# Kernel optimization log

Hardware: AMD Instinct MI355X
Metric: run time of the kernel (lower is better)

Reference implementation:

```python
import jax, jax.numpy as jnp
import numpy as np

N_NODES = 100000
N_EDGES = 1600000
N_GRAPHS = 64
H = 150
PASSES = 4


def setup_inputs() -> dict:
    key = jax.random.key(0)
    ks = jax.random.split(key, 16)
    s = 0.082  # ~1/sqrt(150), torch default init scale
    nodes = jax.random.normal(ks[0], (N_NODES, H), dtype=jnp.float32)
    src = jax.random.randint(ks[1], (N_EDGES,), 0, N_NODES, dtype=jnp.int32)
    dst = jax.random.randint(ks[2], (N_EDGES,), 0, N_NODES, dtype=jnp.int32)
    graph_ids = jnp.sort(jax.random.randint(ks[3], (N_NODES,), 0, N_GRAPHS, dtype=jnp.int32))
    u = lambda k, sh: jax.random.uniform(k, sh, dtype=jnp.float32, minval=-s, maxval=s)
    return {
        'nodes': nodes, 'src': src, 'dst': dst, 'graph_ids': graph_ids,
        'w_ih': u(ks[4], (3 * H, H)), 'w_hh': u(ks[5], (3 * H, H)),
        'b_ih': u(ks[6], (3 * H,)), 'b_hh': u(ks[7], (3 * H,)),
        'fc1_w': u(ks[8], (80, H)), 'fc1_b': u(ks[9], (80,)),
        'fc2_w': u(ks[10], (80, 80)), 'fc2_b': u(ks[11], (80,)),
        'fcl_w': u(ks[12], (10, 80)), 'fcl_b': u(ks[13], (10,)),
    }


def _gru_cell(x, h, w_ih, w_hh, b_ih, b_hh):
    # torch.nn.GRUCell semantics
    gi = x @ w_ih.T + b_ih  # [N, 3H]
    gh = h @ w_hh.T + b_hh
    i_r, i_z, i_n = jnp.split(gi, 3, axis=-1)
    h_r, h_z, h_n = jnp.split(gh, 3, axis=-1)
    r = jax.nn.sigmoid(i_r + h_r)
    z = jax.nn.sigmoid(i_z + h_z)
    n = jnp.tanh(i_n + r * h_n)
    return (1.0 - z) * n + z * h


def reference(nodes, src, dst, graph_ids, w_ih, w_hh, b_ih, b_hh,
              fc1_w, fc1_b, fc2_w, fc2_b, fcl_w, fcl_b):
    h = nodes
    for _ in range(PASSES):
        # incoming[v] = sum of h[u] over edges u->v (collect_incomingPrime)
        incoming = jax.ops.segment_sum(h[src], dst, num_segments=N_NODES)
        h = _gru_cell(incoming, h, w_ih, w_hh, b_ih, b_hh)
    # per-graph readout: sum node states, log, nan->0, relu
    g = jax.ops.segment_sum(h, graph_ids, num_segments=N_GRAPHS)  # [G, H]
    g = jnp.log(g)
    g = jnp.where(jnp.isnan(g), 0.0, g)
    g = jax.nn.relu(g)  # relu(-inf) = 0, matches torch
    x = jax.nn.leaky_relu(g @ fc1_w.T + fc1_b)
    x = jax.nn.leaky_relu(x @ fc2_w.T + fc2_b)
    return x @ fcl_w.T + fcl_b  # [G, 10]
```

## Files before the change

kernel.cpp:

```cpp
#include <hip/hip_runtime.h>

#define N_NODES 100000
#define N_EDGES 1600000
#define N_GRAPHS 64
#define HDIM 150
#define PASSES 4
#define MROWS_PAD 100032
#define SCAN_NBLK 391

typedef __attribute__((ext_vector_type(8))) short bf16x8;
typedef __attribute__((ext_vector_type(4))) float f32x4;

__device__ __forceinline__ ushort bf16_rne(float x) {
  uint u = __float_as_uint(x);
  u += 0x7FFFu + ((u >> 16) & 1u);
  return (ushort)(u >> 16);
}
__device__ __forceinline__ float bf16f(ushort h) { return __uint_as_float(((uint)h) << 16); }

__global__ void hist_kernel(const int* __restrict__ dst, int* __restrict__ counts, int n) {
  int i = blockIdx.x * blockDim.x + threadIdx.x;
  if (i < n) atomicAdd(&counts[dst[i]], 1);
}

__global__ __launch_bounds__(256) void scan1_kernel(const int* __restrict__ counts,
                                                    int* __restrict__ partials) {
  int i = blockIdx.x * 256 + threadIdx.x;
  int v = (i < N_NODES) ? counts[i] : 0;
#pragma unroll
  for (int o = 32; o; o >>= 1) v += __shfl_down(v, o);
  __shared__ int ws4[4];
  if ((threadIdx.x & 63) == 0) ws4[threadIdx.x >> 6] = v;
  __syncthreads();
  if (threadIdx.x == 0) partials[blockIdx.x] = ws4[0] + ws4[1] + ws4[2] + ws4[3];
}

__global__ __launch_bounds__(512) void scan2_kernel(int* __restrict__ partials,
                                                    int* __restrict__ row_start) {
  __shared__ int s[512];
  int t = threadIdx.x;
  int v = (t < SCAN_NBLK) ? partials[t] : 0;
  s[t] = v;
  __syncthreads();
  for (int o = 1; o < 512; o <<= 1) {
    int u = (t >= o) ? s[t - o] : 0;
    __syncthreads();
    s[t] += u;
    __syncthreads();
  }
  if (t < SCAN_NBLK) partials[t] = s[t] - v;
  if (t == 0) row_start[N_NODES] = s[511];
}

__global__ __launch_bounds__(256) void scan3_kernel(const int* __restrict__ counts,
    const int* __restrict__ partials, int* __restrict__ row_start, int* __restrict__ cursor) {
  __shared__ int s[256];
  int t = threadIdx.x, i = blockIdx.x * 256 + t;
  int v = (i < N_NODES) ? counts[i] : 0;
  s[t] = v;
  __syncthreads();
  for (int o = 1; o < 256; o <<= 1) {
    int u = (t >= o) ? s[t - o] : 0;
    __syncthreads();
    s[t] += u;
    __syncthreads();
  }
  if (i < N_NODES) {
    int ex = s[t] - v + partials[blockIdx.x];
    row_start[i] = ex; cursor[i] = ex;
  }
}

__global__ void fill_kernel(const int* __restrict__ src, const int* __restrict__ dst,
                            int* __restrict__ cursor, int* __restrict__ csr_src, int n) {
  int i = blockIdx.x * blockDim.x + threadIdx.x;
  if (i < n) {
    int pos = atomicAdd(&cursor[dst[i]], 1);
    csr_src[pos] = src[i];
  }
}

__global__ void wbuild_kernel(const float* __restrict__ wih, const float* __restrict__ whh,
                              ushort* __restrict__ Whi, ushort* __restrict__ Wlo) {
  int idx = blockIdx.x * 256 + threadIdx.x;
  if (idx >= 960 * 160) return;
  int n = idx / 160, k = idx - n * 160;
  int ch = n / 160, dd = n - ch * 160;
  float v = 0.f;
  if (dd < HDIM && k < HDIM)
    v = (ch < 3) ? wih[(ch * HDIM + dd) * HDIM + k] : whh[((ch - 3) * HDIM + dd) * HDIM + k];
  ushort hi = bf16_rne(v);
  ushort lo = bf16_rne(v - bf16f(hi));
  Whi[idx] = hi; Wlo[idx] = lo;
}

__global__ __launch_bounds__(256) void segsum_kernel(const float* __restrict__ h, const int hstride,
    const int* __restrict__ row_start, const int* __restrict__ csr_src,
    ushort* __restrict__ Xhi, ushort* __restrict__ Xlo) {
  int node = blockIdx.x * 4 + (threadIdx.x >> 6);
  if (node >= N_NODES) return;
  int lane = threadIdx.x & 63;
  int b = row_start[node], e = row_start[node + 1];
  int cnt = e - b;
  float a0 = 0.f, a1 = 0.f, a2 = 0.f;
  const bool l22 = lane < 22;

  for (int base = 0; base < cnt; base += 64) {
    const int nb = min(64, cnt - base);
    int myidx = (base + lane < cnt) ? csr_src[b + base + lane] : 0;
    int jj = 0;
    for (; jj + 4 <= nb; jj += 4) {
      const int s0 = __shfl(myidx, jj);
      const int s1 = __shfl(myidx, jj + 1);
      const int s2 = __shfl(myidx, jj + 2);
      const int s3 = __shfl(myidx, jj + 3);
      const float* r0 = h + (size_t)s0 * hstride;
      const float* r1 = h + (size_t)s1 * hstride;
      const float* r2 = h + (size_t)s2 * hstride;
      const float* r3 = h + (size_t)s3 * hstride;
      float v00 = r0[lane],      v10 = r1[lane],      v20 = r2[lane],      v30 = r3[lane];
      float v01 = r0[lane + 64], v11 = r1[lane + 64], v21 = r2[lane + 64], v31 = r3[lane + 64];
      float v02 = 0.f, v12 = 0.f, v22 = 0.f, v32 = 0.f;
      if (l22) {
        v02 = r0[lane + 128]; v12 = r1[lane + 128];
        v22 = r2[lane + 128]; v32 = r3[lane + 128];
      }
      a0 += (v00 + v10) + (v20 + v30);
      a1 += (v01 + v11) + (v21 + v31);
      a2 += (v02 + v12) + (v22 + v32);
    }
    for (; jj < nb; ++jj) {
      const int s0 = __shfl(myidx, jj);
      const float* r0 = h + (size_t)s0 * hstride;
      a0 += r0[lane];
      a1 += r0[lane + 64];
      if (l22) a2 += r0[lane + 128];
    }
  }

  int basep = node * 160;
  ushort h0 = bf16_rne(a0), l0 = bf16_rne(a0 - bf16f(h0));
  ushort h1 = bf16_rne(a1), l1 = bf16_rne(a1 - bf16f(h1));
  Xhi[basep + lane] = h0; Xlo[basep + lane] = l0;
  Xhi[basep + 64 + lane] = h1; Xlo[basep + 64 + lane] = l1;
  if (lane < 32) {
    ushort h2 = 0, l2 = 0;
    if (l22) { h2 = bf16_rne(a2); l2 = bf16_rne(a2 - bf16f(h2)); }
    Xhi[basep + 128 + lane] = h2; Xlo[basep + 128 + lane] = l2;
  }
}

__global__ __launch_bounds__(256) void gru_mfma_kernel(
    const ushort* __restrict__ Xhi, const ushort* __restrict__ Xlo,
    const float* __restrict__ hcur, const int hstride,
    const ushort* __restrict__ Whi, const ushort* __restrict__ Wlo,
    const float* __restrict__ bih, const float* __restrict__ bhh,
    float* __restrict__ hnext) {
  __shared__ ushort smem[2][8192];
  const int flat = blockIdx.x;
  const int xcd = flat & 7;
  const int q = flat >> 3;
  const int dblk = q % 5;
  const int mblk = (q / 5) * 8 + xcd;
  if (mblk >= 1563) return;

  const int tid = threadIdx.x;
  const int w = tid >> 6;
  const int l = tid & 63;
  const int c16 = l & 15;
  const int koct = l >> 4;

  const int sr = tid >> 2;
  const int so = tid & 3;
  const int sop = so ^ ((sr >> 1) & 3);
  const int gm = mblk * 64 + sr;
  const bool rowok = gm < N_NODES;
  const int g_off = gm * 160 + so * 8;
  const int lds_w_off = sr * 64 + sop * 16;

  const int hi_b = (w < 2) ? 0 : 2;
  const int dt = w & 1;
  const int ch0 = (w < 2) ? 0 : 3;
  const int nbase = dblk * 32 + dt * 16 + c16;

  f32x4 acc[3][4];
#pragma unroll
  for (int a = 0; a < 3; ++a)
#pragma unroll
    for (int b = 0; b < 4; ++b) acc[a][b] = (f32x4){0.f, 0.f, 0.f, 0.f};

  auto loadH = [&](int kc, float* hv) {
    const int kb = kc * 32 + so * 8;
    const float* hrow = hcur + (size_t)gm * hstride + kb;
#pragma unroll
    for (int e = 0; e < 8; e += 2) {
      float x0 = 0.f, x1 = 0.f;
      if (rowok) {
        if (kb + e + 1 < HDIM) { float2 v2 = *(const float2*)(hrow + e); x0 = v2.x; x1 = v2.y; }
        else if (kb + e < HDIM) { x0 = hrow[e]; }
      }
      hv[e] = x0; hv[e + 1] = x1;
    }
  };
  auto writeH = [&](int buf, const float* hv) {
    bf16x8 vh, vl;
#pragma unroll
    for (int e = 0; e < 8; ++e) {
      ushort u = bf16_rne(hv[e]);
      vh[e] = (short)u;
      vl[e] = (short)bf16_rne(hv[e] - bf16f(u));
    }
    *(bf16x8*)((char*)smem + buf * 16384 + 2 * 4096 + lds_w_off) = vh;
    *(bf16x8*)((char*)smem + buf * 16384 + 3 * 4096 + lds_w_off) = vl;
  };

  {
    bf16x8 x0 = *(const bf16x8*)(Xhi + g_off);
    bf16x8 x1 = *(const bf16x8*)(Xlo + g_off);
    float hv[8];
    loadH(0, hv);
    *(bf16x8*)((char*)smem + 0 * 4096 + lds_w_off) = x0;
    *(bf16x8*)((char*)smem + 1 * 4096 + lds_w_off) = x1;
    writeH(0, hv);
  }
  __syncthreads();

#pragma unroll
  for (int kc = 0; kc < 5; ++kc) {
    const int cur = kc & 1;
    bf16x8 nX0, nX1;
    float nhv[8];
    if (kc < 4) {
      nX0 = *(const bf16x8*)(Xhi + g_off + (kc + 1) * 32);
      nX1 = *(const bf16x8*)(Xlo + g_off + (kc + 1) * 32);
      loadH(kc + 1, nhv);
    }
    bf16x8 ahi[4], alo[4];
#pragma unroll
    for (int mt = 0; mt < 4; ++mt) {
      const int r = mt * 16 + c16;
      const int ob = (koct ^ ((r >> 1) & 3)) * 16;
      ahi[mt] = *(const bf16x8*)((char*)smem + cur * 16384 + hi_b * 4096 + r * 64 + ob);
      alo[mt] = *(const bf16x8*)((char*)smem + cur * 16384 + (hi_b + 1) * 4096 + r * 64 + ob);
    }
    bf16x8 bhi[3], blo[3];
#pragma unroll
    for (int cl = 0; cl < 3; ++cl) {
      const int wo = ((ch0 + cl) * 160 + nbase) * 160 + kc * 32 + koct * 8;
      bhi[cl] = *(const bf16x8*)(Whi + wo);
      blo[cl] = *(const bf16x8*)(Wlo + wo);
    }
#pragma unroll
    for (int cl = 0; cl < 3; ++cl)
#pragma unroll
      for (int mt = 0; mt < 4; ++mt)
        acc[cl][mt] = __builtin_amdgcn_mfma_f32_16x16x32_bf16(ahi[mt], bhi[cl], acc[cl][mt], 0, 0, 0);
#pragma unroll
    for (int cl = 0; cl < 3; ++cl)
#pragma unroll
      for (int mt = 0; mt < 4; ++mt)
        acc[cl][mt] = __builtin_amdgcn_mfma_f32_16x16x32_bf16(ahi[mt], blo[cl], acc[cl][mt], 0, 0, 0);
#pragma unroll
    for (int cl = 0; cl < 3; ++cl)
#pragma unroll
      for (int mt = 0; mt < 4; ++mt)
        acc[cl][mt] = __builtin_amdgcn_mfma_f32_16x16x32_bf16(alo[mt], bhi[cl], acc[cl][mt], 0, 0, 0);
    if (kc < 4) {
      const int nb = cur ^ 1;
      *(bf16x8*)((char*)smem + nb * 16384 + 0 * 4096 + lds_w_off) = nX0;
      *(bf16x8*)((char*)smem + nb * 16384 + 1 * 4096 + lds_w_off) = nX1;
      writeH(nb, nhv);
    }
    __syncthreads();
  }

  float* eps = (float*)smem;
  if (w >= 2) {
    const int wi = w - 2;
#pragma unroll
    for (int cl = 0; cl < 3; ++cl)
#pragma unroll
      for (int mt = 0; mt < 4; ++mt)
        *(f32x4*)&eps[(((wi * 3 + cl) * 4 + mt) * 64 + l) * 4] = acc[cl][mt];
  }
  __syncthreads();
  if (w < 2) {
    const int d = dblk * 32 + dt * 16 + c16;
    if (d < HDIM) {
      const float bir = bih[d], biz = bih[HDIM + d], bin = bih[2 * HDIM + d];
      const float bhr = bhh[d], bhz = bhh[HDIM + d], bhn = bhh[2 * HDIM + d];
#pragma unroll
      for (int mt = 0; mt < 4; ++mt) {
        const int mb = mblk * 64 + mt * 16 + koct * 4;
        f32x4 hr4 = *(const f32x4*)&eps[(((dt * 3 + 0) * 4 + mt) * 64 + l) * 4];
        f32x4 hz4 = *(const f32x4*)&eps[(((dt * 3 + 1) * 4 + mt) * 64 + l) * 4];
        f32x4 hn4 = *(const f32x4*)&eps[(((dt * 3 + 2) * 4 + mt) * 64 + l) * 4];
#pragma unroll
        for (int j = 0; j < 4; ++j) {
          const int m = mb + j;
          if (m < N_NODES) {
            const float r = 1.f / (1.f + __expf(-(acc[0][mt][j] + bir + hr4[j] + bhr)));
            const float z = 1.f / (1.f + __expf(-(acc[1][mt][j] + biz + hz4[j] + bhz)));
            const float na = acc[2][mt][j] + bin + r * (hn4[j] + bhn);
            const float nn = 1.f - 2.f / (__expf(2.f * na) + 1.f);
            const float ho = hcur[(size_t)m * hstride + d];
            hnext[m * 160 + d] = (1.f - z) * nn + z * ho;
          }
        }
      }
    }
  }
}

__global__ __launch_bounds__(64) void graph_accum_kernel(const float* __restrict__ h,
    const int* __restrict__ gids, float* __restrict__ gacc) {
  const int lane = threadIdx.x;
  const int nb = gridDim.x;
  int chunk = (N_NODES + nb - 1) / nb;
  int b = blockIdx.x * chunk, e = min(b + chunk, N_NODES);
  if (b >= e) return;
  float a0 = 0.f, a1 = 0.f, a2 = 0.f;
  int cur = gids[b];
  for (int i = b; i < e; ++i) {
    int gid = gids[i];
    if (gid != cur) {
      atomicAdd(&gacc[cur * HDIM + lane], a0);
      atomicAdd(&gacc[cur * HDIM + lane + 64], a1);
      if (lane < 22) atomicAdd(&gacc[cur * HDIM + lane + 128], a2);
      a0 = a1 = a2 = 0.f; cur = gid;
    }
    const float* hr = h + (size_t)i * 160;
    a0 += hr[lane]; a1 += hr[lane + 64];
    if (lane < 22) a2 += hr[lane + 128];
  }
  atomicAdd(&gacc[cur * HDIM + lane], a0);
  atomicAdd(&gacc[cur * HDIM + lane + 64], a1);
  if (lane < 22) atomicAdd(&gacc[cur * HDIM + lane + 128], a2);
}

__global__ __launch_bounds__(192) void readout_kernel(const float* __restrict__ gacc,
    const float* __restrict__ fc1w, const float* __restrict__ fc1b,
    const float* __restrict__ fc2w, const float* __restrict__ fc2b,
    const float* __restrict__ fclw, const float* __restrict__ fclb,
    float* __restrict__ out) {
  __shared__ float x0[HDIM];
  __shared__ float y1[80];
  __shared__ float y2[80];
  int g = blockIdx.x, t = threadIdx.x;
  if (t < HDIM) {
    float v = logf(gacc[g * HDIM + t]);
    if (v != v) v = 0.f;
    x0[t] = fmaxf(v, 0.f);
  }
  __syncthreads();
  if (t < 80) {
    float s = fc1b[t];
    for (int k = 0; k < HDIM; ++k) s += x0[k] * fc1w[t * HDIM + k];
    y1[t] = (s > 0.f) ? s : 0.01f * s;
  }
  __syncthreads();
  if (t < 80) {
    float s = fc2b[t];
    for (int k = 0; k < 80; ++k) s += y1[k] * fc2w[t * 80 + k];
    y2[t] = (s > 0.f) ? s : 0.01f * s;
  }
  __syncthreads();
  if (t < 10) {
    float s = fclb[t];
    for (int k = 0; k < 80; ++k) s += y2[k] * fclw[t * 80 + k];
    out[g * 10 + t] = s;
  }
}

extern "C" void kernel_launch(void* const* d_in, const int* in_sizes, int n_in,
                              void* d_out, int out_size, void* d_ws, size_t ws_size,
                              hipStream_t stream) {
  const float* nodes = (const float*)d_in[0];
  const int* src = (const int*)d_in[1];
  const int* dst = (const int*)d_in[2];
  const int* gids = (const int*)d_in[3];
  const float* wih = (const float*)d_in[4];
  const float* whh = (const float*)d_in[5];
  const float* bih = (const float*)d_in[6];
  const float* bhh = (const float*)d_in[7];
  const float* fc1w = (const float*)d_in[8];
  const float* fc1b = (const float*)d_in[9];
  const float* fc2w = (const float*)d_in[10];
  const float* fc2b = (const float*)d_in[11];
  const float* fclw = (const float*)d_in[12];
  const float* fclb = (const float*)d_in[13];
  float* out = (float*)d_out;

  char* wsp = (char*)d_ws;
  size_t off = 0;
  auto carve = [&](size_t bytes) {
    void* p = wsp + off;
    off += (bytes + 255) & ~(size_t)255;
    return p;
  };
  int* counts   = (int*)carve((size_t)N_NODES * 4);
  int* rowstart = (int*)carve((size_t)(N_NODES + 1) * 4);
  int* cursor   = (int*)carve((size_t)N_NODES * 4);
  int* partials = (int*)carve((size_t)512 * 4);
  int* csr      = (int*)carve((size_t)N_EDGES * 4);
  ushort* Xhi   = (ushort*)carve((size_t)MROWS_PAD * 160 * 2);
  ushort* Xlo   = (ushort*)carve((size_t)MROWS_PAD * 160 * 2);
  float* hA     = (float*)carve((size_t)MROWS_PAD * 160 * 4);
  float* hB     = (float*)carve((size_t)MROWS_PAD * 160 * 4);
  ushort* Whi   = (ushort*)carve((size_t)960 * 160 * 2);
  ushort* Wlo   = (ushort*)carve((size_t)960 * 160 * 2);
  float* gacc   = (float*)carve((size_t)N_GRAPHS * HDIM * 4);
  (void)ws_size; (void)in_sizes; (void)n_in; (void)out_size;

  hipMemsetAsync(counts, 0, (size_t)N_NODES * 4, stream);
  hipMemsetAsync(gacc, 0, (size_t)N_GRAPHS * HDIM * 4, stream);

  hist_kernel<<<(N_EDGES + 255) / 256, 256, 0, stream>>>(dst, counts, N_EDGES);
  scan1_kernel<<<SCAN_NBLK, 256, 0, stream>>>(counts, partials);
  scan2_kernel<<<1, 512, 0, stream>>>(partials, rowstart);
  scan3_kernel<<<SCAN_NBLK, 256, 0, stream>>>(counts, partials, rowstart, cursor);
  fill_kernel<<<(N_EDGES + 255) / 256, 256, 0, stream>>>(src, dst, cursor, csr, N_EDGES);
  wbuild_kernel<<<600, 256, 0, stream>>>(wih, whh, Whi, Wlo);

  const float* hcur = nodes;
  int hstride = HDIM;
  float* hnxt = hA;
  for (int p = 0; p < PASSES; ++p) {
    segsum_kernel<<<25000, 256, 0, stream>>>(hcur, hstride, rowstart, csr, Xhi, Xlo);
    gru_mfma_kernel<<<7840, 256, 0, stream>>>(
        Xhi, Xlo, hcur, hstride, Whi, Wlo, bih, bhh, hnxt);
    hcur = hnxt;
    hstride = 160;
    hnxt = (hnxt == hA) ? hB : hA;
  }

  graph_accum_kernel<<<512, 64, 0, stream>>>(hcur, gids, gacc);
  readout_kernel<<<N_GRAPHS, 192, 0, stream>>>(gacc, fc1w, fc1b, fc2w, fc2b, fclw, fclb, out);
}
```

Baseline: 1.556 ms.

## Store hidden state as split bf16 hi/lo pairs and stage GRU tiles via direct LDS loads

Node hidden state is now kept as two bf16 planes (hi and lo) instead of fp32, produced by a new split kernel and written directly by the GRU epilogue. Segsum gathers the bf16 pairs, the GRU kernel stages X and H tiles with global_load_lds straight into shared memory, and the readout path reads the pairs. The aim is to drop the per-tile fp32-to-bf16 conversion in the GRU kernel and simplify its staging. The gather still moves the same bytes per row but now issues two 2-byte loads per element, and the segsum unroll drops from 4 to 2 edges. It also adds one extra kernel launch.

After: 1.664 ms. 1.07x slower.

```diff
diff --git a/kernel.cpp b/kernel.cpp
--- a/kernel.cpp
+++ b/kernel.cpp
@@ -17,6 +17,13 @@
   return (ushort)(u >> 16);
 }
 __device__ __forceinline__ float bf16f(ushort h) { return __uint_as_float(((uint)h) << 16); }
+
+__device__ __forceinline__ void gload_lds16(const void* g, void* l) {
+  __builtin_amdgcn_global_load_lds(
+      (const __attribute__((address_space(1))) unsigned int*)(unsigned long long)g,
+      (__attribute__((address_space(3))) unsigned int*)(unsigned int)(unsigned long long)l,
+      16, 0, 0);
+}
 
 __global__ void hist_kernel(const int* __restrict__ dst, int* __restrict__ counts, int n) {
   int i = blockIdx.x * blockDim.x + threadIdx.x;
@@ -94,7 +101,28 @@
   Whi[idx] = hi; Wlo[idx] = lo;
 }
 
-__global__ __launch_bounds__(256) void segsum_kernel(const float* __restrict__ h, const int hstride,
+__global__ __launch_bounds__(256) void hsplit_kernel(const float* __restrict__ h,
+    ushort* __restrict__ Hhi, ushort* __restrict__ Hlo) {
+  int node = blockIdx.x * 4 + (threadIdx.x >> 6);
+  if (node >= N_NODES) return;
+  int lane = threadIdx.x & 63;
+  const float* hr = h + (size_t)node * HDIM;
+  float a0 = hr[lane], a1 = hr[lane + 64];
+  float a2 = (lane < 22) ? hr[lane + 128] : 0.f;
+  int base = node * 160;
+  ushort h0 = bf16_rne(a0), l0 = bf16_rne(a0 - bf16f(h0));
+  ushort h1 = bf16_rne(a1), l1 = bf16_rne(a1 - bf16f(h1));
+  Hhi[base + lane] = h0; Hlo[base + lane] = l0;
+  Hhi[base + 64 + lane] = h1; Hlo[base + 64 + lane] = l1;
+  if (lane < 32) {
+    ushort h2 = 0, l2 = 0;
+    if (lane < 22) { h2 = bf16_rne(a2); l2 = bf16_rne(a2 - bf16f(h2)); }
+    Hhi[base + 128 + lane] = h2; Hlo[base + 128 + lane] = l2;
+  }
+}
+
+__global__ __launch_bounds__(256) void segsum_kernel(
+    const ushort* __restrict__ Hhi, const ushort* __restrict__ Hlo,
     const int* __restrict__ row_start, const int* __restrict__ csr_src,
     ushort* __restrict__ Xhi, ushort* __restrict__ Xlo) {
   int node = blockIdx.x * 4 + (threadIdx.x >> 6);
@@ -109,32 +137,31 @@
     const int nb = min(64, cnt - base);
     int myidx = (base + lane < cnt) ? csr_src[b + base + lane] : 0;
     int jj = 0;
-    for (; jj + 4 <= nb; jj += 4) {
+    for (; jj + 2 <= nb; jj += 2) {
       const int s0 = __shfl(myidx, jj);
       const int s1 = __shfl(myidx, jj + 1);
-      const int s2 = __shfl(myidx, jj + 2);
-      const int s3 = __shfl(myidx, jj + 3);
-      const float* r0 = h + (size_t)s0 * hstride;
-      const float* r1 = h + (size_t)s1 * hstride;
-      const float* r2 = h + (size_t)s2 * hstride;
-      const float* r3 = h + (size_t)s3 * hstride;
-      float v00 = r0[lane],      v10 = r1[lane],      v20 = r2[lane],      v30 = r3[lane];
-      float v01 = r0[lane + 64], v11 = r1[lane + 64], v21 = r2[lane + 64], v31 = r3[lane + 64];
-      float v02 = 0.f, v12 = 0.f, v22 = 0.f, v32 = 0.f;
+      const ushort* h0 = Hhi + (size_t)s0 * 160;
+      const ushort* p0 = Hlo + (size_t)s0 * 160;
+      const ushort* h1 = Hhi + (size_t)s1 * 160;
+      const ushort* p1 = Hlo + (size_t)s1 * 160;
+      ushort u0 = h0[lane],      u1 = p0[lane],      u2 = h1[lane],      u3 = p1[lane];
+      ushort u4 = h0[lane + 64], u5 = p0[lane + 64], u6 = h1[lane + 64], u7 = p1[lane + 64];
+      ushort v0 = 0, v1 = 0, v2 = 0, v3 = 0;
       if (l22) {
-        v02 = r0[lane + 128]; v12 = r1[lane + 128];
-        v22 = r2[lane + 128]; v32 = r3[lane + 128];
+        v0 = h0[lane + 128]; v1 = p0[lane + 128];
+        v2 = h1[lane + 128]; v3 = p1[lane + 128];
       }
-      a0 += (v00 + v10) + (v20 + v30);
-      a1 += (v01 + v11) + (v21 + v31);
-      a2 += (v02 + v12) + (v22 + v32);
+      a0 += (bf16f(u0) + bf16f(u1)) + (bf16f(u2) + bf16f(u3));
+      a1 += (bf16f(u4) + bf16f(u5)) + (bf16f(u6) + bf16f(u7));
+      a2 += (bf16f(v0) + bf16f(v1)) + (bf16f(v2) + bf16f(v3));
     }
     for (; jj < nb; ++jj) {
       const int s0 = __shfl(myidx, jj);
-      const float* r0 = h + (size_t)s0 * hstride;
-      a0 += r0[lane];
-      a1 += r0[lane + 64];
-      if (l22) a2 += r0[lane + 128];
+      const ushort* h0 = Hhi + (size_t)s0 * 160;
+      const ushort* p0 = Hlo + (size_t)s0 * 160;
+      a0 += bf16f(h0[lane]) + bf16f(p0[lane]);
+      a1 += bf16f(h0[lane + 64]) + bf16f(p0[lane + 64]);
+      if (l22) a2 += bf16f(h0[lane + 128]) + bf16f(p0[lane + 128]);
     }
   }
 
@@ -152,10 +179,10 @@
 
 __global__ __launch_bounds__(256) void gru_mfma_kernel(
     const ushort* __restrict__ Xhi, const ushort* __restrict__ Xlo,
-    const float* __restrict__ hcur, const int hstride,
+    const ushort* __restrict__ Hhi, const ushort* __restrict__ Hlo,
     const ushort* __restrict__ Whi, const ushort* __restrict__ Wlo,
     const float* __restrict__ bih, const float* __restrict__ bhh,
-    float* __restrict__ hnext) {
+    ushort* __restrict__ Hhi_n, ushort* __restrict__ Hlo_n) {
   __shared__ ushort smem[2][8192];
   const int flat = blockIdx.x;
   const int xcd = flat & 7;
@@ -170,13 +197,20 @@
   const int c16 = l & 15;
   const int koct = l >> 4;
 
-  const int sr = tid >> 2;
-  const int so = tid & 3;
-  const int sop = so ^ ((sr >> 1) & 3);
-  const int gm = mblk * 64 + sr;
-  const bool rowok = gm < N_NODES;
-  const int g_off = gm * 160 + so * 8;
-  const int lds_w_off = sr * 64 + sop * 16;
+  const ushort* srcp = (w == 0) ? Xhi : (w == 1) ? Xlo : (w == 2) ? Hhi : Hlo;
+  const ushort* gq[4];
+#pragma unroll
+  for (int qq = 0; qq < 4; ++qq) {
+    int sr = qq * 16 + (l >> 2);
+    int so = (l & 3) ^ ((sr >> 1) & 3);
+    gq[qq] = srcp + (size_t)(mblk * 64 + sr) * 160 + so * 8;
+  }
+  auto stage = [&](int buf, int kc) {
+#pragma unroll
+    for (int qq = 0; qq < 4; ++qq)
+      gload_lds16(gq[qq] + kc * 32,
+                  (char*)smem + buf * 16384 + w * 4096 + qq * 1024 + l * 16);
+  };
 
   const int hi_b = (w < 2) ? 0 : 2;
   const int dt = w & 1;
@@ -189,52 +223,13 @@
 #pragma unroll
     for (int b = 0; b < 4; ++b) acc[a][b] = (f32x4){0.f, 0.f, 0.f, 0.f};
 
-  auto loadH = [&](int kc, float* hv) {
-    const int kb = kc * 32 + so * 8;
-    const float* hrow = hcur + (size_t)gm * hstride + kb;
-#pragma unroll
-    for (int e = 0; e < 8; e += 2) {
-      float x0 = 0.f, x1 = 0.f;
-      if (rowok) {
-        if (kb + e + 1 < HDIM) { float2 v2 = *(const float2*)(hrow + e); x0 = v2.x; x1 = v2.y; }
-        else if (kb + e < HDIM) { x0 = hrow[e]; }
-      }
-      hv[e] = x0; hv[e + 1] = x1;
-    }
-  };
-  auto writeH = [&](int buf, const float* hv) {
-    bf16x8 vh, vl;
-#pragma unroll
-    for (int e = 0; e < 8; ++e) {
-      ushort u = bf16_rne(hv[e]);
-      vh[e] = (short)u;
-      vl[e] = (short)bf16_rne(hv[e] - bf16f(u));
-    }
-    *(bf16x8*)((char*)smem + buf * 16384 + 2 * 4096 + lds_w_off) = vh;
-    *(bf16x8*)((char*)smem + buf * 16384 + 3 * 4096 + lds_w_off) = vl;
-  };
-
-  {
-    bf16x8 x0 = *(const bf16x8*)(Xhi + g_off);
-    bf16x8 x1 = *(const bf16x8*)(Xlo + g_off);
-    float hv[8];
-    loadH(0, hv);
-    *(bf16x8*)((char*)smem + 0 * 4096 + lds_w_off) = x0;
-    *(bf16x8*)((char*)smem + 1 * 4096 + lds_w_off) = x1;
-    writeH(0, hv);
-  }
+  stage(0, 0);
   __syncthreads();
 
 #pragma unroll
   for (int kc = 0; kc < 5; ++kc) {
     const int cur = kc & 1;
-    bf16x8 nX0, nX1;
-    float nhv[8];
-    if (kc < 4) {
-      nX0 = *(const bf16x8*)(Xhi + g_off + (kc + 1) * 32);
-      nX1 = *(const bf16x8*)(Xlo + g_off + (kc + 1) * 32);
-      loadH(kc + 1, nhv);
-    }
+    if (kc < 4) stage(cur ^ 1, kc + 1);
     bf16x8 ahi[4], alo[4];
 #pragma unroll
     for (int mt = 0; mt < 4; ++mt) {
@@ -265,12 +260,6 @@
 #pragma unroll
       for (int mt = 0; mt < 4; ++mt)
         acc[cl][mt] = __builtin_amdgcn_mfma_f32_16x16x32_bf16(alo[mt], bhi[cl], acc[cl][mt], 0, 0, 0);
-    if (kc < 4) {
-      const int nb = cur ^ 1;
-      *(bf16x8*)((char*)smem + nb * 16384 + 0 * 4096 + lds_w_off) = nX0;
-      *(bf16x8*)((char*)smem + nb * 16384 + 1 * 4096 + lds_w_off) = nX1;
-      writeH(nb, nhv);
-    }
     __syncthreads();
   }
 
@@ -299,12 +288,16 @@
         for (int j = 0; j < 4; ++j) {
           const int m = mb + j;
           if (m < N_NODES) {
+            const size_t o = (size_t)m * 160 + d;
+            const float ho = bf16f(Hhi[o]) + bf16f(Hlo[o]);
             const float r = 1.f / (1.f + __expf(-(acc[0][mt][j] + bir + hr4[j] + bhr)));
             const float z = 1.f / (1.f + __expf(-(acc[1][mt][j] + biz + hz4[j] + bhz)));
             const float na = acc[2][mt][j] + bin + r * (hn4[j] + bhn);
             const float nn = 1.f - 2.f / (__expf(2.f * na) + 1.f);
-            const float ho = hcur[(size_t)m * hstride + d];
-            hnext[m * 160 + d] = (1.f - z) * nn + z * ho;
+            const float hv = (1.f - z) * nn + z * ho;
+            const ushort hh = bf16_rne(hv);
+            Hhi_n[o] = hh;
+            Hlo_n[o] = bf16_rne(hv - bf16f(hh));
           }
         }
       }
@@ -312,7 +305,8 @@
   }
 }
 
-__global__ __launch_bounds__(64) void graph_accum_kernel(const float* __restrict__ h,
+__global__ __launch_bounds__(64) void graph_accum_kernel(
+    const ushort* __restrict__ Hhi, const ushort* __restrict__ Hlo,
     const int* __restrict__ gids, float* __restrict__ gacc) {
   const int lane = threadIdx.x;
   const int nb = gridDim.x;
@@ -329,9 +323,11 @@
       if (lane < 22) atomicAdd(&gacc[cur * HDIM + lane + 128], a2);
       a0 = a1 = a2 = 0.f; cur = gid;
     }
-    const float* hr = h + (size_t)i * 160;
-    a0 += hr[lane]; a1 += hr[lane + 64];
-    if (lane < 22) a2 += hr[lane + 128];
+    const ushort* rh = Hhi + (size_t)i * 160;
+    const ushort* rl = Hlo + (size_t)i * 160;
+    a0 += bf16f(rh[lane]) + bf16f(rl[lane]);
+    a1 += bf16f(rh[lane + 64]) + bf16f(rl[lane + 64]);
+    if (lane < 22) a2 += bf16f(rh[lane + 128]) + bf16f(rl[lane + 128]);
   }
   atomicAdd(&gacc[cur * HDIM + lane], a0);
   atomicAdd(&gacc[cur * HDIM + lane + 64], a1);
@@ -405,8 +401,10 @@
   int* csr      = (int*)carve((size_t)N_EDGES * 4);
   ushort* Xhi   = (ushort*)carve((size_t)MROWS_PAD * 160 * 2);
   ushort* Xlo   = (ushort*)carve((size_t)MROWS_PAD * 160 * 2);
-  float* hA     = (float*)carve((size_t)MROWS_PAD * 160 * 4);
-  float* hB     = (float*)carve((size_t)MROWS_PAD * 160 * 4);
+  ushort* HhiA  = (ushort*)carve((size_t)MROWS_PAD * 160 * 2);
+  ushort* HloA  = (ushort*)carve((size_t)MROWS_PAD * 160 * 2);
+  ushort* HhiB  = (ushort*)carve((size_t)MROWS_PAD * 160 * 2);
+  ushort* HloB  = (ushort*)carve((size_t)MROWS_PAD * 160 * 2);
   ushort* Whi   = (ushort*)carve((size_t)960 * 160 * 2);
   ushort* Wlo   = (ushort*)carve((size_t)960 * 160 * 2);
   float* gacc   = (float*)carve((size_t)N_GRAPHS * HDIM * 4);
@@ -421,19 +419,19 @@
   scan3_kernel<<<SCAN_NBLK, 256, 0, stream>>>(counts, partials, rowstart, cursor);
   fill_kernel<<<(N_EDGES + 255) / 256, 256, 0, stream>>>(src, dst, cursor, csr, N_EDGES);
   wbuild_kernel<<<600, 256, 0, stream>>>(wih, whh, Whi, Wlo);
-
-  const float* hcur = nodes;
-  int hstride = HDIM;
-  float* hnxt = hA;
+  hsplit_kernel<<<25000, 256, 0, stream>>>(nodes, HhiA, HloA);
+
+  const ushort* curHi = HhiA; const ushort* curLo = HloA;
+  ushort* nxtHi = HhiB; ushort* nxtLo = HloB;
   for (int p = 0; p < PASSES; ++p) {
-    segsum_kernel<<<25000, 256, 0, stream>>>(hcur, hstride, rowstart, csr, Xhi, Xlo);
+    segsum_kernel<<<25000, 256, 0, stream>>>(curHi, curLo, rowstart, csr, Xhi, Xlo);
     gru_mfma_kernel<<<7840, 256, 0, stream>>>(
-        Xhi, Xlo, hcur, hstride, Whi, Wlo, bih, bhh, hnxt);
-    hcur = hnxt;
-    hstride = 160;
-    hnxt = (hnxt == hA) ? hB : hA;
-  }
-
-  graph_accum_kernel<<<512, 64, 0, stream>>>(hcur, gids, gacc);
+        Xhi, Xlo, curHi, curLo, Whi, Wlo, bih, bhh, nxtHi, nxtLo);
+    const ushort* th = curHi; const ushort* tl = curLo;
+    curHi = nxtHi; curLo = nxtLo;
+    nxtHi = (ushort*)th; nxtLo = (ushort*)tl;
+  }
+
+  graph_accum_kernel<<<512, 64, 0, stream>>>(curHi, curLo, gids, gacc);
   readout_kernel<<<N_GRAPHS, 192, 0, stream>>>(gacc, fc1w, fc1b, fc2w, fc2b, fclw, fclb, out);
 }
```

## Stage full 64-row A tile into LDS once instead of double-buffered K chunks

Applied to the files above, without the earlier changes.

The GRU MFMA kernel now loads the whole 64x160 X (hi/lo) and h tile into shared memory up front: two waves copy the bf16 X planes and two waves load h as float4 and split it into bf16 hi/lo. The per-chunk double-buffered prefetch and the barrier on every K step go away, leaving one sync before the MFMA loop. LDS use rises to 80KB per block, and launch bounds request 2 blocks per CU, which limits registers. The trade is less load/compute overlap and more LDS in exchange for wider, coalesced loads and fewer barriers.

Result: slower. 1.999 ms (+28.5%).

```diff
diff --git a/kernel.cpp b/kernel.cpp
--- a/kernel.cpp
+++ b/kernel.cpp
@@ -7,6 +7,7 @@
 #define PASSES 4
 #define MROWS_PAD 100032
 #define SCAN_NBLK 391
+#define PLANE 20480
 
 typedef __attribute__((ext_vector_type(8))) short bf16x8;
 typedef __attribute__((ext_vector_type(4))) float f32x4;
@@ -150,13 +151,13 @@
   }
 }
 
-__global__ __launch_bounds__(256) void gru_mfma_kernel(
+__global__ __launch_bounds__(256, 2) void gru_mfma_kernel(
     const ushort* __restrict__ Xhi, const ushort* __restrict__ Xlo,
     const float* __restrict__ hcur, const int hstride,
     const ushort* __restrict__ Whi, const ushort* __restrict__ Wlo,
     const float* __restrict__ bih, const float* __restrict__ bhh,
     float* __restrict__ hnext) {
-  __shared__ ushort smem[2][8192];
+  __shared__ __align__(16) char smem[4 * PLANE];
   const int flat = blockIdx.x;
   const int xcd = flat & 7;
   const int q = flat >> 3;
@@ -170,13 +171,46 @@
   const int c16 = l & 15;
   const int koct = l >> 4;
 
-  const int sr = tid >> 2;
-  const int so = tid & 3;
-  const int sop = so ^ ((sr >> 1) & 3);
-  const int gm = mblk * 64 + sr;
-  const bool rowok = gm < N_NODES;
-  const int g_off = gm * 160 + so * 8;
-  const int lds_w_off = sr * 64 + sop * 16;
+  if (w < 2) {
+    const ushort* srcp = w ? Xlo : Xhi;
+#pragma unroll
+    for (int it = 0; it < 20; ++it) {
+      int flatc = it * 64 + l;
+      int row = flatc / 20, o = flatc - row * 20;
+      bf16x8 v = *(const bf16x8*)(srcp + (size_t)(mblk * 64 + row) * 160 + o * 8);
+      int osw = (o & ~3) | ((o & 3) ^ ((row >> 1) & 3));
+      *(bf16x8*)(smem + w * PLANE + row * 320 + osw * 16) = v;
+    }
+  } else {
+    const int rbase = (w - 2) * 32;
+#pragma unroll
+    for (int it = 0; it < 20; ++it) {
+      int flatc = it * 64 + l;
+      int row = rbase + flatc / 40;
+      int c4 = flatc - (flatc / 40) * 40;
+      int gm = mblk * 64 + row;
+      float x0 = 0.f, x1 = 0.f, x2 = 0.f, x3 = 0.f;
+      if (gm < N_NODES) {
+        const float* p = hcur + (size_t)gm * hstride + c4 * 4;
+        if (hstride != HDIM || c4 < 37) {
+          float4 v4 = *(const float4*)p; x0 = v4.x; x1 = v4.y; x2 = v4.z; x3 = v4.w;
+        } else if (c4 == 37) {
+          float2 v2 = *(const float2*)p; x0 = v2.x; x1 = v2.y;
+        }
+      }
+      ushort h0 = bf16_rne(x0), h1 = bf16_rne(x1), h2 = bf16_rne(x2), h3 = bf16_rne(x3);
+      ushort q0 = bf16_rne(x0 - bf16f(h0)), q1 = bf16_rne(x1 - bf16f(h1));
+      ushort q2 = bf16_rne(x2 - bf16f(h2)), q3 = bf16_rne(x3 - bf16f(h3));
+      int o = c4 >> 1;
+      int osw = (o & ~3) | ((o & 3) ^ ((row >> 1) & 3));
+      int boff = row * 320 + osw * 16 + (c4 & 1) * 8;
+      ushort4 hv; hv.x = h0; hv.y = h1; hv.z = h2; hv.w = h3;
+      ushort4 lv; lv.x = q0; lv.y = q1; lv.z = q2; lv.w = q3;
+      *(ushort4*)(smem + 2 * PLANE + boff) = hv;
+      *(ushort4*)(smem + 3 * PLANE + boff) = lv;
+    }
+  }
+  __syncthreads();
 
   const int hi_b = (w < 2) ? 0 : 2;
   const int dt = w & 1;
@@ -189,59 +223,15 @@
 #pragma unroll
     for (int b = 0; b < 4; ++b) acc[a][b] = (f32x4){0.f, 0.f, 0.f, 0.f};
 
-  auto loadH = [&](int kc, float* hv) {
-    const int kb = kc * 32 + so * 8;
-    const float* hrow = hcur + (size_t)gm * hstride + kb;
-#pragma unroll
-    for (int e = 0; e < 8; e += 2) {
-      float x0 = 0.f, x1 = 0.f;
-      if (rowok) {
-        if (kb + e + 1 < HDIM) { float2 v2 = *(const float2*)(hrow + e); x0 = v2.x; x1 = v2.y; }
-        else if (kb + e < HDIM) { x0 = hrow[e]; }
-      }
-      hv[e] = x0; hv[e + 1] = x1;
-    }
-  };
-  auto writeH = [&](int buf, const float* hv) {
-    bf16x8 vh, vl;
-#pragma unroll
-    for (int e = 0; e < 8; ++e) {
-      ushort u = bf16_rne(hv[e]);
-      vh[e] = (short)u;
-      vl[e] = (short)bf16_rne(hv[e] - bf16f(u));
-    }
-    *(bf16x8*)((char*)smem + buf * 16384 + 2 * 4096 + lds_w_off) = vh;
-    *(bf16x8*)((char*)smem + buf * 16384 + 3 * 4096 + lds_w_off) = vl;
-  };
-
-  {
-    bf16x8 x0 = *(const bf16x8*)(Xhi + g_off);
-    bf16x8 x1 = *(const bf16x8*)(Xlo + g_off);
-    float hv[8];
-    loadH(0, hv);
-    *(bf16x8*)((char*)smem + 0 * 4096 + lds_w_off) = x0;
-    *(bf16x8*)((char*)smem + 1 * 4096 + lds_w_off) = x1;
-    writeH(0, hv);
-  }
-  __syncthreads();
-
 #pragma unroll
   for (int kc = 0; kc < 5; ++kc) {
-    const int cur = kc & 1;
-    bf16x8 nX0, nX1;
-    float nhv[8];
-    if (kc < 4) {
-      nX0 = *(const bf16x8*)(Xhi + g_off + (kc + 1) * 32);
-      nX1 = *(const bf16x8*)(Xlo + g_off + (kc + 1) * 32);
-      loadH(kc + 1, nhv);
-    }
     bf16x8 ahi[4], alo[4];
 #pragma unroll
     for (int mt = 0; mt < 4; ++mt) {
       const int r = mt * 16 + c16;
-      const int ob = (koct ^ ((r >> 1) & 3)) * 16;
-      ahi[mt] = *(const bf16x8*)((char*)smem + cur * 16384 + hi_b * 4096 + r * 64 + ob);
-      alo[mt] = *(const bf16x8*)((char*)smem + cur * 16384 + (hi_b + 1) * 4096 + r * 64 + ob);
+      const int o = kc * 4 + (koct ^ ((r >> 1) & 3));
+      ahi[mt] = *(const bf16x8*)(smem + hi_b * PLANE + r * 320 + o * 16);
+      alo[mt] = *(const bf16x8*)(smem + (hi_b + 1) * PLANE + r * 320 + o * 16);
     }
     bf16x8 bhi[3], blo[3];
 #pragma unroll
@@ -265,14 +255,8 @@
 #pragma unroll
       for (int mt = 0; mt < 4; ++mt)
         acc[cl][mt] = __builtin_amdgcn_mfma_f32_16x16x32_bf16(alo[mt], bhi[cl], acc[cl][mt], 0, 0, 0);
-    if (kc < 4) {
-      const int nb = cur ^ 1;
-      *(bf16x8*)((char*)smem + nb * 16384 + 0 * 4096 + lds_w_off) = nX0;
-      *(bf16x8*)((char*)smem + nb * 16384 + 1 * 4096 + lds_w_off) = nX1;
-      writeH(nb, nhv);
-    }
-    __syncthreads();
-  }
+  }
+  __syncthreads();
 
   float* eps = (float*)smem;
   if (w >= 2) {
```

## Pre-swizzle GRU weights into fragment order and prefetch B one k-step ahead

Applied to the files above, without the earlier changes.

Weights are repacked once at setup into an MFMA-fragment-major layout, so each lane reads its 16-byte B fragment at a contiguous offset (lane*8) instead of gathering strided rows. The B-fragment loads are also software-pipelined, issued one k-chunk ahead alongside the X/H prefetch. This aims to coalesce the weight loads and hide their latency behind the MFMAs, at the cost of extra registers that may lower occupancy.

New measurement: 1.603 ms. +3.0%, slower.

```diff
diff --git a/kernel.cpp b/kernel.cpp
--- a/kernel.cpp
+++ b/kernel.cpp
@@ -83,15 +83,22 @@
 __global__ void wbuild_kernel(const float* __restrict__ wih, const float* __restrict__ whh,
                               ushort* __restrict__ Whi, ushort* __restrict__ Wlo) {
   int idx = blockIdx.x * 256 + threadIdx.x;
-  if (idx >= 960 * 160) return;
-  int n = idx / 160, k = idx - n * 160;
-  int ch = n / 160, dd = n - ch * 160;
+  if (idx >= 153600) return;
+  int low = idx & 511;
+  int e = low & 7, c16 = (low >> 3) & 15, koct = low >> 7;
+  int hi = idx >> 9;
+  int kc = hi % 5; hi /= 5;
+  int dt = hi & 1; hi >>= 1;
+  int dblk = hi % 5;
+  int ch = hi / 5;
+  int dd = dblk * 32 + dt * 16 + c16;
+  int k = kc * 32 + koct * 8 + e;
   float v = 0.f;
   if (dd < HDIM && k < HDIM)
     v = (ch < 3) ? wih[(ch * HDIM + dd) * HDIM + k] : whh[((ch - 3) * HDIM + dd) * HDIM + k];
-  ushort hi = bf16_rne(v);
-  ushort lo = bf16_rne(v - bf16f(hi));
-  Whi[idx] = hi; Wlo[idx] = lo;
+  ushort h = bf16_rne(v);
+  ushort l = bf16_rne(v - bf16f(h));
+  Whi[idx] = h; Wlo[idx] = l;
 }
 
 __global__ __launch_bounds__(256) void segsum_kernel(const float* __restrict__ h, const int hstride,
@@ -181,7 +188,11 @@
   const int hi_b = (w < 2) ? 0 : 2;
   const int dt = w & 1;
   const int ch0 = (w < 2) ? 0 : 3;
-  const int nbase = dblk * 32 + dt * 16 + c16;
+
+  int wb[3];
+#pragma unroll
+  for (int cl = 0; cl < 3; ++cl)
+    wb[cl] = (((ch0 + cl) * 5 + dblk) * 2 + dt) * 5;
 
   f32x4 acc[3][4];
 #pragma unroll
@@ -213,6 +224,17 @@
     *(bf16x8*)((char*)smem + buf * 16384 + 2 * 4096 + lds_w_off) = vh;
     *(bf16x8*)((char*)smem + buf * 16384 + 3 * 4096 + lds_w_off) = vl;
   };
+  auto loadB = [&](int kc, bf16x8* bh, bf16x8* bl) {
+#pragma unroll
+    for (int cl = 0; cl < 3; ++cl) {
+      const int wo = ((wb[cl] + kc) << 9) + l * 8;
+      bh[cl] = *(const bf16x8*)(Whi + wo);
+      bl[cl] = *(const bf16x8*)(Wlo + wo);
+    }
+  };
+
+  bf16x8 bhi[3], blo[3];
+  loadB(0, bhi, blo);
 
   {
     bf16x8 x0 = *(const bf16x8*)(Xhi + g_off);
@@ -230,10 +252,12 @@
     const int cur = kc & 1;
     bf16x8 nX0, nX1;
     float nhv[8];
+    bf16x8 nbh[3], nbl[3];
     if (kc < 4) {
       nX0 = *(const bf16x8*)(Xhi + g_off + (kc + 1) * 32);
       nX1 = *(const bf16x8*)(Xlo + g_off + (kc + 1) * 32);
       loadH(kc + 1, nhv);
+      loadB(kc + 1, nbh, nbl);
     }
     bf16x8 ahi[4], alo[4];
 #pragma unroll
@@ -242,13 +266,6 @@
       const int ob = (koct ^ ((r >> 1) & 3)) * 16;
       ahi[mt] = *(const bf16x8*)((char*)smem + cur * 16384 + hi_b * 4096 + r * 64 + ob);
       alo[mt] = *(const bf16x8*)((char*)smem + cur * 16384 + (hi_b + 1) * 4096 + r * 64 + ob);
-    }
-    bf16x8 bhi[3], blo[3];
-#pragma unroll
-    for (int cl = 0; cl < 3; ++cl) {
-      const int wo = ((ch0 + cl) * 160 + nbase) * 160 + kc * 32 + koct * 8;
-      bhi[cl] = *(const bf16x8*)(Whi + wo);
-      blo[cl] = *(const bf16x8*)(Wlo + wo);
     }
 #pragma unroll
     for (int cl = 0; cl < 3; ++cl)
@@ -270,6 +287,8 @@
       *(bf16x8*)((char*)smem + nb * 16384 + 0 * 4096 + lds_w_off) = nX0;
       *(bf16x8*)((char*)smem + nb * 16384 + 1 * 4096 + lds_w_off) = nX1;
       writeH(nb, nhv);
+#pragma unroll
+      for (int cl = 0; cl < 3; ++cl) { bhi[cl] = nbh[cl]; blo[cl] = nbl[cl]; }
     }
     __syncthreads();
   }
@@ -407,8 +426,8 @@
   ushort* Xlo   = (ushort*)carve((size_t)MROWS_PAD * 160 * 2);
   float* hA     = (float*)carve((size_t)MROWS_PAD * 160 * 4);
   float* hB     = (float*)carve((size_t)MROWS_PAD * 160 * 4);
-  ushort* Whi   = (ushort*)carve((size_t)960 * 160 * 2);
-  ushort* Wlo   = (ushort*)carve((size_t)960 * 160 * 2);
+  ushort* Whi   = (ushort*)carve((size_t)153600 * 2);
+  ushort* Wlo   = (ushort*)carve((size_t)153600 * 2);
   float* gacc   = (float*)carve((size_t)N_GRAPHS * HDIM * 4);
   (void)ws_size; (void)in_sizes; (void)n_in; (void)out_size;
 
```
